# Kernel optimization log

Measured on AMD Instinct MI355X. Metric: run time of the kernel, lower is better.

The kernel has to match this reference:

```python
import jax, jax.numpy as jnp
import numpy as np

NEG_INF = -1e38


def wkv(k, v, w, u):
    """Log-sum-exp-stabilized RWKV WKV scan.
    k, v: (B, T, C); w, u: (C,). Returns y: (B, T, C).
    """
    B, T, C = k.shape

    def step(carry, kv_t):
        num, den, mx = carry            # each (B, C)
        k_t, v_t = kv_t                 # (B, C)
        ku = k_t + u
        m = jnp.maximum(mx, ku)
        e1 = jnp.exp(mx - m)
        e2 = jnp.exp(ku - m)
        y = (e1 * num + e2 * v_t) / (e1 * den + e2)
        # state update
        mw = mx + w
        m2 = jnp.maximum(mw, k_t)
        es1 = jnp.exp(mw - m2)
        es2 = jnp.exp(k_t - m2)
        num = es1 * num + es2 * v_t
        den = es1 * den + es2
        return (num, den, m2), y

    init = (jnp.zeros((B, C), k.dtype),
            jnp.zeros((B, C), k.dtype),
            jnp.full((B, C), NEG_INF, k.dtype))
    _, y = jax.lax.scan(step, init, (jnp.swapaxes(k, 0, 1), jnp.swapaxes(v, 0, 1)))
    return jnp.swapaxes(y, 0, 1)


def setup_inputs() -> dict:
    key = jax.random.key(0)
    ks = jax.random.split(key, 8)
    B, T, C = 8, 4096, 512
    x = jax.random.normal(ks[0], (B, T, C), dtype=jnp.float32)
    # Linear weights stored as (in, out) so forward is x @ W.
    W_rkv = jax.random.normal(ks[1], (C, 6 * C), dtype=jnp.float32) / np.sqrt(C)
    W_out = jax.random.normal(ks[2], (2 * C, C), dtype=jnp.float32) / np.sqrt(2 * C)
    time_decay = jax.random.uniform(ks[3], (C,), minval=-6.0, maxval=-5.0, dtype=jnp.float32)
    time_first = jax.random.uniform(ks[4], (C,), minval=-3.0, maxval=0.0, dtype=jnp.float32)
    time_decay_rev = jax.random.uniform(ks[5], (C,), minval=-6.0, maxval=-5.0, dtype=jnp.float32)
    time_first_rev = jax.random.uniform(ks[6], (C,), minval=-3.0, maxval=0.0, dtype=jnp.float32)
    return {"x": x, "W_rkv": W_rkv, "W_out": W_out,
            "time_decay": time_decay, "time_first": time_first,
            "time_decay_rev": time_decay_rev, "time_first_rev": time_first_rev}


def reference(x, W_rkv, W_out, time_decay, time_first, time_decay_rev, time_first_rev):
    B, T, C = x.shape
    rkv = (x @ W_rkv).reshape(B, T, 2, 3, C)
    # forward direction
    r_f, k_f, v_f = rkv[:, :, 0, 0], rkv[:, :, 0, 1], rkv[:, :, 0, 2]
    w_f = -jnp.exp(time_decay)
    out_f = jax.nn.sigmoid(r_f) * wkv(k_f, v_f, w_f, time_first)
    # backward direction (run scan on time-reversed k/v, then reverse back)
    r_b, k_b, v_b = rkv[:, :, 1, 0], rkv[:, :, 1, 1], rkv[:, :, 1, 2]
    w_b = -jnp.exp(time_decay_rev)
    out_b = wkv(k_b[:, ::-1], v_b[:, ::-1], w_b, time_first_rev)[:, ::-1]
    out_b = jax.nn.sigmoid(r_b) * out_b
    out_cat = jnp.concatenate([out_f, out_b], axis=-1)  # (B, T, 2C)
    return out_cat @ W_out
```

## Files before the change

### kernel.cpp

```cpp
#include <hip/hip_runtime.h>

typedef float f4 __attribute__((ext_vector_type(4)));
typedef unsigned short us4 __attribute__((ext_vector_type(4)));
typedef __bf16 bf16x8 __attribute__((ext_vector_type(8)));
typedef float f32x4 __attribute__((ext_vector_type(4)));
typedef _Float16 h8 __attribute__((ext_vector_type(8)));

#define TT 4096
#define CCH 512
#define NCH2 256
#define CHL2 16
#define NSEG 32
#define SEGC 8

__device__ __forceinline__ unsigned short f2bf(float f) {
  unsigned u = __builtin_bit_cast(unsigned, f);
  unsigned r = (u + 0x7FFFu + ((u >> 16) & 1u)) >> 16;
  return (unsigned short)r;
}
__device__ __forceinline__ void gload_lds16(const void* g, void* l) {
  __builtin_amdgcn_global_load_lds(
      (const __attribute__((address_space(1))) unsigned int*)g,
      (__attribute__((address_space(3))) unsigned int*)l, 16, 0, 0);
}
#define VMCNT(n) asm volatile("s_waitcnt vmcnt(" #n ")" ::: "memory")

__global__ __launch_bounds__(256)
void convert_f32_bf16(const float* __restrict__ in, unsigned short* __restrict__ out, int n4) {
  int i = blockIdx.x * 256 + threadIdx.x;
  if (i >= n4) return;
  f4 f = *(const f4*)(in + (size_t)i * 4);
  us4 o = { f2bf(f[0]), f2bf(f[1]), f2bf(f[2]), f2bf(f[3]) };
  *(us4*)(out + (size_t)i * 4) = o;
}

__global__ __launch_bounds__(256)
void transpose_to_bf16(const float* __restrict__ in, unsigned short* __restrict__ out,
                       int R, int Cc) {
  __shared__ unsigned short tile[32][33];
  int c0 = blockIdx.x * 32, r0 = blockIdx.y * 32;
  int tx = threadIdx.x, ty = threadIdx.y;
  #pragma unroll
  for (int j = 0; j < 32; j += 8)
    tile[ty + j][tx] = f2bf(in[(size_t)(r0 + ty + j) * Cc + c0 + tx]);
  __syncthreads();
  #pragma unroll
  for (int j = 0; j < 32; j += 8)
    out[(size_t)(c0 + ty + j) * R + r0 + tx] = tile[tx][ty + j];
}

__global__ __launch_bounds__(256)
void transpose_to_f16(const float* __restrict__ in, _Float16* __restrict__ out,
                      int R, int Cc) {
  __shared__ _Float16 tile[32][33];
  int c0 = blockIdx.x * 32, r0 = blockIdx.y * 32;
  int tx = threadIdx.x, ty = threadIdx.y;
  #pragma unroll
  for (int j = 0; j < 32; j += 8)
    tile[ty + j][tx] = (_Float16)in[(size_t)(r0 + ty + j) * Cc + c0 + tx];
  __syncthreads();
  #pragma unroll
  for (int j = 0; j < 32; j += 8)
    out[(size_t)(c0 + ty + j) * R + r0 + tx] = tile[tx][ty + j];
}

__global__ __launch_bounds__(512, 2)
void gemm256_g1(const unsigned short* __restrict__ A,
                const unsigned short* __restrict__ BT,
                _Float16* __restrict__ kbuf, _Float16* __restrict__ vbuf,
                _Float16* __restrict__ rbuf) {
  __shared__ char lds[131072];
  const int tid = threadIdx.x;
  const int lane = tid & 63, wv = tid >> 6;
  const int wm = wv >> 2, wn = wv & 3;
  const int ln15 = lane & 15, lq = lane >> 4;

  const int nwg = gridDim.x;
  const int bid = blockIdx.x;
  const int wgid = (nwg % 8 == 0) ? (bid % 8) * (nwg / 8) + bid / 8 : bid;
  const int bn = wgid % 12, bm = wgid / 12;
  const size_t m0 = (size_t)bm * 256, n0 = (size_t)bn * 256;
  const char* Ab = (const char*)(A + m0 * 512);
  const char* Bb = (const char*)(BT + n0 * 512);

  const int srow0 = tid >> 2, srow1 = 128 + (tid >> 2);
  const int sg = tid & 3;
  const int sgs0 = (sg ^ ((srow0 >> 1) & 3)) << 4;
  const int sgs1 = (sg ^ ((srow1 >> 1) & 3)) << 4;

  auto STAGE = [&](int mat, int t, int h) {
    const char* gsrc = mat ? Bb : Ab;
    char* ldst = lds + mat * 65536 + ((t & 1) << 15) + (h << 14);
    const size_t co = (size_t)t * 128 + (size_t)h * 64;
    gload_lds16(gsrc + (size_t)srow0 * 1024 + co + sgs0, ldst + tid * 16);
    gload_lds16(gsrc + (size_t)srow1 * 1024 + co + sgs1, ldst + 8192 + tid * 16);
  };

  f32x4 acc[8][4] = {};
  STAGE(0, 0, 0); STAGE(1, 0, 0); STAGE(0, 0, 1); STAGE(1, 0, 1);

  for (int t = 0; t < 8; ++t) {
    char* Abase = lds + ((t & 1) << 15);
    char* Bbase = lds + 65536 + ((t & 1) << 15);
    VMCNT(4);
    __builtin_amdgcn_s_barrier();
    __builtin_amdgcn_sched_barrier(0);
    {
      bf16x8 bf[4], af[8];
      #pragma unroll
      for (int fn = 0; fn < 4; ++fn) {
        const int r = wn * 64 + fn * 16 + ln15;
        bf[fn] = *(const bf16x8*)(Bbase + r * 64 + ((lq ^ ((r >> 1) & 3)) << 4));
      }
      #pragma unroll
      for (int fm = 0; fm < 8; ++fm) {
        const int r = wm * 128 + fm * 16 + ln15;
        af[fm] = *(const bf16x8*)(Abase + r * 64 + ((lq ^ ((r >> 1) & 3)) << 4));
      }
      if (t < 7) { STAGE(0, t + 1, 0); STAGE(1, t + 1, 0); }
      __builtin_amdgcn_s_setprio(1);
      #pragma unroll
      for (int fm = 0; fm < 8; ++fm)
        #pragma unroll
        for (int fn = 0; fn < 4; ++fn)
          acc[fm][fn] = __builtin_amdgcn_mfma_f32_16x16x32_bf16(af[fm], bf[fn], acc[fm][fn], 0, 0, 0);
      __builtin_amdgcn_s_setprio(0);
    }
    if (t < 7) { VMCNT(4); } else { VMCNT(0); }
    __builtin_amdgcn_s_barrier();
    __builtin_amdgcn_sched_barrier(0);
    {
      bf16x8 bf[4], af[8];
      #pragma unroll
      for (int fn = 0; fn < 4; ++fn) {
        const int r = wn * 64 + fn * 16 + ln15;
        bf[fn] = *(const bf16x8*)(Bbase + 16384 + r * 64 + ((lq ^ ((r >> 1) & 3)) << 4));
      }
      #pragma unroll
      for (int fm = 0; fm < 8; ++fm) {
        const int r = wm * 128 + fm * 16 + ln15;
        af[fm] = *(const bf16x8*)(Abase + 16384 + r * 64 + ((lq ^ ((r >> 1) & 3)) << 4));
      }
      if (t < 7) { STAGE(0, t + 1, 1); STAGE(1, t + 1, 1); }
      __builtin_amdgcn_s_setprio(1);
      #pragma unroll
      for (int fm = 0; fm < 8; ++fm)
        #pragma unroll
        for (int fn = 0; fn < 4; ++fn)
          acc[fm][fn] = __builtin_amdgcn_mfma_f32_16x16x32_bf16(af[fm], bf[fn], acc[fm][fn], 0, 0, 0);
      __builtin_amdgcn_s_setprio(0);
    }
  }

  const int n0i = (int)n0;
  const int dir = (n0i >= 1536) ? 1 : 0;
  const int jj0 = n0i - dir * 1536;
  const int seg = jj0 >> 9;
  const int cbase = jj0 & 511;
  _Float16* dbuf = (seg == 0) ? rbuf : (seg == 1 ? kbuf : vbuf);
  float* stg = (float*)lds;
  const int ebnd = wv >> 2;
  const int erow = (tid >> 3) & 31;
  const int el8 = tid & 7;
  __syncthreads();
  #pragma unroll
  for (int gi = 0; gi < 4; ++gi) {
    #pragma unroll
    for (int f2 = 0; f2 < 2; ++f2) {
      const int fm = gi * 2 + f2;
      #pragma unroll
      for (int q = 0; q < 4; ++q) {
        const int rloc = f2 * 16 + lq * 4 + q;
        float* dst = stg + wm * 8192 + rloc * 256;
        const int sw = ((rloc >> 2) & 1) << 4;
        #pragma unroll
        for (int fn = 0; fn < 4; ++fn)
          dst[(wn * 64 + fn * 16 + ln15) ^ sw] = acc[fm][fn][q];
      }
    }
    __syncthreads();
    {
      const int rowg = (int)m0 + ebnd * 128 + gi * 32 + erow;
      const int b_ = rowg >> 12, tt = rowg & 4095;
      const int trow = dir ? (4095 - tt) : tt;
      _Float16* gp = dbuf + ((size_t)(b_ * 2 + dir) * TT + trow) * 512 + cbase;
      const float* sp = stg + ebnd * 8192 + erow * 256;
      const int sw = ((erow >> 2) & 1) << 4;
      #pragma unroll
      for (int u = 0; u < 4; ++u) {
        const int cf = el8 * 8 + u * 64;
        const int cs = cf ^ sw;
        f4 a = *(const f4*)(sp + cs);
        f4 b = *(const f4*)(sp + cs + 4);
        h8 hv = { (_Float16)a[0], (_Float16)a[1], (_Float16)a[2], (_Float16)a[3],
                  (_Float16)b[0], (_Float16)b[1], (_Float16)b[2], (_Float16)b[3] };
        *(h8*)(gp + cf) = hv;
      }
    }
    __syncthreads();
  }
}

__global__ __launch_bounds__(256)
void gemm2_k(const _Float16* __restrict__ obuf,
             const _Float16* __restrict__ BT,
             int M, float* __restrict__ out) {
  __shared__ char smem[16384];
  _Float16* As  = (_Float16*)smem;
  _Float16* Bsm = (_Float16*)(smem + 8192);
  const int tid = threadIdx.x;
  const int lane = tid & 63, wv = tid >> 6;
  const int wr = wv >> 1, wc = wv & 1;
  const int ln15 = lane & 15, lq = lane >> 4;
  const int mtiles = M >> 7;
  const int bm = blockIdx.x % mtiles, bn = blockIdx.x / mtiles;
  const size_t m0 = (size_t)bm << 7, n0 = (size_t)bn << 7;
  f32x4 acc[4][4] = {};
  const int bB = (int)(m0 >> 12);
  const int tbase = (int)(m0 & 4095);
  const char* Bb = (const char*)(BT + n0 * 1024);
  const int r0 = tid >> 2;
  const int cb = (((tid & 3) ^ (r0 & 3)) << 4);

  for (int k0 = 0; k0 < 1024; k0 += 32) {
    const int half = k0 >> 9;
    const size_t kb = (size_t)(k0 & 511) * 2;
    const char* Ah = (const char*)(obuf + ((size_t)(bB * 2 + half) << 12) * 512);
    const size_t ar0 = half ? (size_t)(4095 - (tbase + r0))      : (size_t)(tbase + r0);
    const size_t ar1 = half ? (size_t)(4095 - (tbase + r0 + 64)) : (size_t)(tbase + r0 + 64);
    gload_lds16(Ah + ar0 * 1024 + kb + cb, (char*)As + tid * 16);
    gload_lds16(Ah + ar1 * 1024 + kb + cb, (char*)As + 4096 + tid * 16);
    gload_lds16(Bb + (size_t)r0 * 2048 + (size_t)k0 * 2 + cb,        (char*)Bsm + tid * 16);
    gload_lds16(Bb + (size_t)(r0 + 64) * 2048 + (size_t)k0 * 2 + cb, (char*)Bsm + 4096 + tid * 16);
    __syncthreads();
    h8 af[4], bg[4];
    #pragma unroll
    for (int i = 0; i < 4; ++i) {
      const int ar = wr * 64 + i * 16 + ln15;
      const int br = wc * 64 + i * 16 + ln15;
      af[i] = *(const h8*)((char*)As  + ((ar * 4 + (lq ^ (ar & 3))) << 4));
      bg[i] = *(const h8*)((char*)Bsm + ((br * 4 + (lq ^ (br & 3))) << 4));
    }
    #pragma unroll
    for (int i = 0; i < 4; ++i)
      #pragma unroll
      for (int j = 0; j < 4; ++j)
        acc[i][j] = __builtin_amdgcn_mfma_f32_16x16x32_f16(af[i], bg[j], acc[i][j], 0, 0, 0);
    __syncthreads();
  }

  const int tq = tid >> 3, t8 = tid & 7;
  #pragma unroll
  for (int i = 0; i < 4; ++i) {
    __syncthreads();
    float* st = (float*)smem;
    #pragma unroll
    for (int j = 0; j < 4; ++j) {
      const int cl = wc * 64 + j * 16 + ln15;
      #pragma unroll
      for (int q = 0; q < 4; ++q) {
        const int rl = wr * 16 + lq * 4 + q;
        st[rl * 128 + (cl ^ (((rl >> 2) & 3) << 4))] = acc[i][j][q];
      }
    }
    __syncthreads();
    const int rl = tq, lqp = (rl >> 2) & 3;
    const int lr = ((rl >> 4) << 6) + (i << 4) + (rl & 15);
    const int rowg = (int)m0 + lr;
    #pragma unroll
    for (int u = 0; u < 4; ++u) {
      const int colL = t8 * 16 + u * 4;
      const int colS = colL ^ (lqp << 4);
      f4 vv = *(const f4*)(st + rl * 128 + colS);
      *(f4*)(out + (size_t)rowg * 512 + n0 + colL) = vv;
    }
  }
}

__global__ __launch_bounds__(128)
void wkv_pass1(const _Float16* __restrict__ kbuf, const _Float16* __restrict__ vbuf,
               const float* __restrict__ td, const float* __restrict__ tdr,
               float* __restrict__ cN, float* __restrict__ cD, float* __restrict__ cM) {
  const int bd = blockIdx.x;
  const int ch = blockIdx.y * 2 + threadIdx.y;
  const int dir = bd & 1;
  const int c = threadIdx.x * 8;
  const float* tdp = (dir ? tdr : td) + c;
  float w[8], num[8], den[8], m[8];
  #pragma unroll
  for (int e = 0; e < 8; ++e) { w[e] = -__expf(tdp[e]); num[e] = 0.f; den[e] = 0.f; m[e] = -1e38f; }
  const size_t base = ((size_t)bd * TT + (size_t)ch * CHL2) * CCH + c;
  const _Float16* kp = kbuf + base;
  const _Float16* vp = vbuf + base;
  h8 ka = *(const h8*)(kp), va = *(const h8*)(vp);
  h8 kb = *(const h8*)(kp + CCH), vb = *(const h8*)(vp + CCH);
  for (int t = 0; t < CHL2; ++t) {
    h8 kc = {}, vc = {};
    if (t + 2 < CHL2) {
      kc = *(const h8*)(kp + (size_t)(t + 2) * CCH);
      vc = *(const h8*)(vp + (size_t)(t + 2) * CCH);
    }
    #pragma unroll
    for (int e = 0; e < 8; ++e) {
      float ke = (float)ka[e], ve = (float)va[e];
      float mw = m[e] + w[e];
      float m2 = fmaxf(mw, ke);
      float e1 = __expf(mw - m2), e2 = __expf(ke - m2);
      num[e] = e1 * num[e] + e2 * ve;
      den[e] = e1 * den[e] + e2;
      m[e] = m2;
    }
    ka = kb; va = vb; kb = kc; vb = vc;
  }
  const size_t ci = ((size_t)bd * NCH2 + ch) * CCH + c;
  #pragma unroll
  for (int h = 0; h < 2; ++h) {
    *(f4*)(cN + ci + h * 4) = (f4){num[h*4], num[h*4+1], num[h*4+2], num[h*4+3]};
    *(f4*)(cD + ci + h * 4) = (f4){den[h*4], den[h*4+1], den[h*4+2], den[h*4+3]};
    *(f4*)(cM + ci + h * 4) = (f4){m[h*4], m[h*4+1], m[h*4+2], m[h*4+3]};
  }
}

__global__ __launch_bounds__(128)
void wkv_p2a(const float* __restrict__ td, const float* __restrict__ tdr,
             const float* __restrict__ cN, const float* __restrict__ cD,
             const float* __restrict__ cM,
             float* __restrict__ scN, float* __restrict__ scD, float* __restrict__ scM) {
  const int bd = blockIdx.x, seg = blockIdx.y;
  const int dir = bd & 1;
  const int c = threadIdx.x * 4;
  f4 tdv = *(const f4*)((dir ? tdr : td) + c);
  float dw[4], num[4], den[4], m[4];
  #pragma unroll
  for (int e = 0; e < 4; ++e) { dw[e] = -__expf(tdv[e]) * (float)CHL2; num[e] = 0.f; den[e] = 0.f; m[e] = -1e38f; }
  size_t ci = ((size_t)bd * NCH2 + (size_t)seg * SEGC) * CCH + c;
  for (int j = 0; j < SEGC; ++j, ci += CCH) {
    f4 ln = *(const f4*)(cN + ci);
    f4 ld = *(const f4*)(cD + ci);
    f4 lm = *(const f4*)(cM + ci);
    #pragma unroll
    for (int e = 0; e < 4; ++e) {
      float mp = m[e] + dw[e];
      float mm = fmaxf(mp, lm[e]);
      float e1 = __expf(mp - mm), e2 = __expf(lm[e] - mm);
      num[e] = e1 * num[e] + e2 * ln[e];
      den[e] = e1 * den[e] + e2 * ld[e];
      m[e] = mm;
    }
  }
  const size_t si = ((size_t)bd * NSEG + seg) * CCH + c;
  *(f4*)(scN + si) = (f4){num[0], num[1], num[2], num[3]};
  *(f4*)(scD + si) = (f4){den[0], den[1], den[2], den[3]};
  *(f4*)(scM + si) = (f4){m[0], m[1], m[2], m[3]};
}

__global__ __launch_bounds__(128)
void wkv_p2b(const float* __restrict__ td, const float* __restrict__ tdr,
             float* __restrict__ scN, float* __restrict__ scD, float* __restrict__ scM) {
  const int bd = blockIdx.x;
  const int dir = bd & 1;
  const int c = threadIdx.x * 4;
  f4 tdv = *(const f4*)((dir ? tdr : td) + c);
  float dws[4], num[4], den[4], m[4];
  #pragma unroll
  for (int e = 0; e < 4; ++e) { dws[e] = -__expf(tdv[e]) * (float)(CHL2 * SEGC); num[e] = 0.f; den[e] = 0.f; m[e] = -1e38f; }
  size_t si = (size_t)bd * NSEG * CCH + c;
  for (int s = 0; s < NSEG; ++s, si += CCH) {
    f4 ln = *(const f4*)(scN + si);
    f4 ld = *(const f4*)(scD + si);
    f4 lm = *(const f4*)(scM + si);
    *(f4*)(scN + si) = (f4){num[0], num[1], num[2], num[3]};
    *(f4*)(scD + si) = (f4){den[0], den[1], den[2], den[3]};
    *(f4*)(scM + si) = (f4){m[0], m[1], m[2], m[3]};
    #pragma unroll
    for (int e = 0; e < 4; ++e) {
      float mp = m[e] + dws[e];
      float mm = fmaxf(mp, lm[e]);
      float e1 = __expf(mp - mm), e2 = __expf(lm[e] - mm);
      num[e] = e1 * num[e] + e2 * ln[e];
      den[e] = e1 * den[e] + e2 * ld[e];
      m[e] = mm;
    }
  }
}

__global__ __launch_bounds__(128)
void wkv_p2c(const float* __restrict__ td, const float* __restrict__ tdr,
             const float* __restrict__ scN, const float* __restrict__ scD,
             const float* __restrict__ scM,
             float* __restrict__ cN, float* __restrict__ cD, float* __restrict__ cM) {
  const int bd = blockIdx.x, seg = blockIdx.y;
  const int dir = bd & 1;
  const int c = threadIdx.x * 4;
  f4 tdv = *(const f4*)((dir ? tdr : td) + c);
  const size_t si = ((size_t)bd * NSEG + seg) * CCH + c;
  f4 nv = *(const f4*)(scN + si);
  f4 dv = *(const f4*)(scD + si);
  f4 mv = *(const f4*)(scM + si);
  float dw[4], num[4], den[4], m[4];
  #pragma unroll
  for (int e = 0; e < 4; ++e) {
    dw[e] = -__expf(tdv[e]) * (float)CHL2;
    num[e] = nv[e]; den[e] = dv[e]; m[e] = mv[e];
  }
  size_t ci = ((size_t)bd * NCH2 + (size_t)seg * SEGC) * CCH + c;
  for (int j = 0; j < SEGC; ++j, ci += CCH) {
    f4 ln = *(const f4*)(cN + ci);
    f4 ld = *(const f4*)(cD + ci);
    f4 lm = *(const f4*)(cM + ci);
    *(f4*)(cN + ci) = (f4){num[0], num[1], num[2], num[3]};
    *(f4*)(cD + ci) = (f4){den[0], den[1], den[2], den[3]};
    *(f4*)(cM + ci) = (f4){m[0], m[1], m[2], m[3]};
    #pragma unroll
    for (int e = 0; e < 4; ++e) {
      float mp = m[e] + dw[e];
      float mm = fmaxf(mp, lm[e]);
      float e1 = __expf(mp - mm), e2 = __expf(lm[e] - mm);
      num[e] = e1 * num[e] + e2 * ln[e];
      den[e] = e1 * den[e] + e2 * ld[e];
      m[e] = mm;
    }
  }
}

__global__ __launch_bounds__(128)
void wkv_pass3(const _Float16* __restrict__ kbuf, const _Float16* __restrict__ vbuf,
               _Float16* __restrict__ rbuf,
               const float* __restrict__ td, const float* __restrict__ tf,
               const float* __restrict__ tdr, const float* __restrict__ tfr,
               const float* __restrict__ cN, const float* __restrict__ cD,
               const float* __restrict__ cM) {
  const int bd = blockIdx.x;
  const int ch = blockIdx.y * 2 + threadIdx.y;
  const int dir = bd & 1;
  const int c = threadIdx.x * 8;
  const float* tdp = (dir ? tdr : td) + c;
  const float* tup = (dir ? tfr : tf) + c;
  const size_t ci = ((size_t)bd * NCH2 + ch) * CCH + c;
  float w[8], u[8], num[8], den[8], m[8];
  #pragma unroll
  for (int e = 0; e < 8; ++e) {
    w[e] = -__expf(tdp[e]); u[e] = tup[e];
    num[e] = cN[ci + e]; den[e] = cD[ci + e]; m[e] = cM[ci + e];
  }
  const size_t base = ((size_t)bd * TT + (size_t)ch * CHL2) * CCH + c;
  const _Float16* kp = kbuf + base;
  const _Float16* vp = vbuf + base;
  _Float16* rp = rbuf + base;
  h8 ka = *(const h8*)(kp), va = *(const h8*)(vp), ra = *(const h8*)(rp);
  h8 kb = *(const h8*)(kp + CCH), vb = *(const h8*)(vp + CCH), rb = *(const h8*)(rp + CCH);
  for (int t = 0; t < CHL2; ++t) {
    h8 kc = {}, vc = {}, rc = {};
    if (t + 2 < CHL2) {
      kc = *(const h8*)(kp + (size_t)(t + 2) * CCH);
      vc = *(const h8*)(vp + (size_t)(t + 2) * CCH);
      rc = *(const h8*)(rp + (size_t)(t + 2) * CCH);
    }
    _Float16 o[8];
    #pragma unroll
    for (int e = 0; e < 8; ++e) {
      float ke = (float)ka[e], ve = (float)va[e];
      float ku = ke + u[e];
      float mm = fmaxf(m[e], ku);
      float e1 = __expf(m[e] - mm), e2 = __expf(ku - mm);
      float y = (e1 * num[e] + e2 * ve) * __builtin_amdgcn_rcpf(e1 * den[e] + e2);
      float rt = (float)ra[e];
      float sig = __builtin_amdgcn_rcpf(1.f + __expf(-rt));
      o[e] = (_Float16)(sig * y);
      float mw = m[e] + w[e];
      float m2 = fmaxf(mw, ke);
      float es1 = __expf(mw - m2), es2 = __expf(ke - m2);
      num[e] = es1 * num[e] + es2 * ve;
      den[e] = es1 * den[e] + es2;
      m[e] = m2;
    }
    h8 ov = { o[0], o[1], o[2], o[3], o[4], o[5], o[6], o[7] };
    *(h8*)(rp + (size_t)t * CCH) = ov;
    ka = kb; va = vb; ra = rb; kb = kc; vb = vc; rb = rc;
  }
}

extern "C" void kernel_launch(void* const* d_in, const int* in_sizes, int n_in,
                              void* d_out, int out_size, void* d_ws, size_t ws_size,
                              hipStream_t stream) {
  const float* x   = (const float*)d_in[0];
  const float* Wr  = (const float*)d_in[1];
  const float* Wo  = (const float*)d_in[2];
  const float* td  = (const float*)d_in[3];
  const float* tf  = (const float*)d_in[4];
  const float* tdr = (const float*)d_in[5];
  const float* tfr = (const float*)d_in[6];
  float* out = (float*)d_out;

  auto rnd = [](size_t b) { return (b + 255) & ~(size_t)255; };
  const size_t wBytes = rnd((size_t)3072 * 512 * 2) + rnd((size_t)512 * 1024 * 2);
  auto need = [&](int Bs) {
    size_t s = wBytes;
    s += 3 * rnd((size_t)Bs * 2 * TT * 512 * 2);
    s += rnd((size_t)Bs * TT * 512 * 2);
    return s;
  };
  int Bs = 8;
  while (Bs > 1 && need(Bs) > ws_size) Bs >>= 1;

  char* ws = (char*)d_ws;
  size_t off = 0;
  auto alloc = [&](size_t bytes) -> char* {
    char* p = ws + off;
    off += (bytes + 255) & ~(size_t)255;
    return p;
  };
  unsigned short* wrkvT = (unsigned short*)alloc((size_t)3072 * 512 * 2);
  _Float16*       woutT = (_Float16*)alloc((size_t)512 * 1024 * 2);
  _Float16*       kbuf  = (_Float16*)alloc((size_t)Bs * 2 * TT * 512 * 2);
  _Float16*       vbuf  = (_Float16*)alloc((size_t)Bs * 2 * TT * 512 * 2);
  _Float16*       rbuf  = (_Float16*)alloc((size_t)Bs * 2 * TT * 512 * 2);
  unsigned short* xb    = (unsigned short*)alloc((size_t)Bs * TT * 512 * 2);
  const size_t cs = (size_t)Bs * 2 * NCH2 * 512;
  const size_t ss = (size_t)Bs * 2 * NSEG * 512;
  float* cN  = (float*)xb;
  float* cD  = cN + cs;
  float* cM  = cD + cs;
  float* scN = cM + cs;
  float* scD = scN + ss;
  float* scM = scD + ss;

  transpose_to_bf16<<<dim3(3072 / 32, 512 / 32), dim3(32, 8), 0, stream>>>(Wr, wrkvT, 512, 3072);
  transpose_to_f16<<<dim3(512 / 32, 1024 / 32), dim3(32, 8), 0, stream>>>(Wo, woutT, 1024, 512);

  const int nslices = 8 / Bs;
  const int Mslice = Bs * TT;
  const int mt256 = Mslice >> 8;
  const int mt128 = Mslice >> 7;
  for (int s = 0; s < nslices; ++s) {
    const float* xs = x + (size_t)s * Mslice * 512;
    float* outs = out + (size_t)s * Mslice * 512;
    convert_f32_bf16<<<Mslice * 512 / 1024, 256, 0, stream>>>(xs, xb, Mslice * 512 / 4);
    gemm256_g1<<<mt256 * 12, 512, 0, stream>>>(xb, wrkvT, kbuf, vbuf, rbuf);
    wkv_pass1<<<dim3(Bs * 2, NCH2 / 2), dim3(64, 2), 0, stream>>>(kbuf, vbuf, td, tdr, cN, cD, cM);
    wkv_p2a<<<dim3(Bs * 2, NSEG), 128, 0, stream>>>(td, tdr, cN, cD, cM, scN, scD, scM);
    wkv_p2b<<<Bs * 2, 128, 0, stream>>>(td, tdr, scN, scD, scM);
    wkv_p2c<<<dim3(Bs * 2, NSEG), 128, 0, stream>>>(td, tdr, scN, scD, scM, cN, cD, cM);
    wkv_pass3<<<dim3(Bs * 2, NCH2 / 2), dim3(64, 2), 0, stream>>>(kbuf, vbuf, rbuf, td, tf, tdr, tfr,
                                                                  cN, cD, cM);
    gemm2_k<<<mt128 * 4, 256, 0, stream>>>(rbuf, woutT, Mslice, outs);
  }
}
```

Baseline: 334.3 us.

## Replace output GEMM with 256x256 tile, double-buffered LDS pipelined kernel

Replaces the 128x128 single-buffered output projection GEMM with a 256x256-tile, 512-thread kernel. It stages 64-wide K chunks in two halves, double-buffers them in LDS, and overlaps global-to-LDS loads with MFMA using vmcnt waits and s_setprio. It also remaps workgroup IDs so neighbouring blocks land on different XCDs, and uses a wider swizzled epilogue. The aim is more data reuse per tile and less load latency exposed in the K loop. The cost is 128KB of LDS and heavy register use, which limits occupancy. The grid also becomes small (two N tiles), which may underfill the CUs.

```diff
diff --git a/kernel.cpp b/kernel.cpp
--- a/kernel.cpp
+++ b/kernel.cpp
@@ -201,79 +201,140 @@
   }
 }
 
-__global__ __launch_bounds__(256)
-void gemm2_k(const _Float16* __restrict__ obuf,
-             const _Float16* __restrict__ BT,
-             int M, float* __restrict__ out) {
-  __shared__ char smem[16384];
-  _Float16* As  = (_Float16*)smem;
-  _Float16* Bsm = (_Float16*)(smem + 8192);
+__global__ __launch_bounds__(512, 2)
+void gemm2_256(const _Float16* __restrict__ obuf,
+               const _Float16* __restrict__ BT,
+               float* __restrict__ out) {
+  __shared__ char lds[131072];
   const int tid = threadIdx.x;
   const int lane = tid & 63, wv = tid >> 6;
-  const int wr = wv >> 1, wc = wv & 1;
+  const int wm = wv >> 2, wn = wv & 3;
   const int ln15 = lane & 15, lq = lane >> 4;
-  const int mtiles = M >> 7;
-  const int bm = blockIdx.x % mtiles, bn = blockIdx.x / mtiles;
-  const size_t m0 = (size_t)bm << 7, n0 = (size_t)bn << 7;
-  f32x4 acc[4][4] = {};
+
+  const int nwg = gridDim.x;
+  const int bid = blockIdx.x;
+  const int wgid = (nwg % 8 == 0) ? (bid % 8) * (nwg / 8) + bid / 8 : bid;
+  const int bn = wgid % 2, bm = wgid / 2;
+  const size_t m0 = (size_t)bm * 256, n0 = (size_t)bn * 256;
   const int bB = (int)(m0 >> 12);
   const int tbase = (int)(m0 & 4095);
   const char* Bb = (const char*)(BT + n0 * 1024);
-  const int r0 = tid >> 2;
-  const int cb = (((tid & 3) ^ (r0 & 3)) << 4);
-
-  for (int k0 = 0; k0 < 1024; k0 += 32) {
-    const int half = k0 >> 9;
-    const size_t kb = (size_t)(k0 & 511) * 2;
-    const char* Ah = (const char*)(obuf + ((size_t)(bB * 2 + half) << 12) * 512);
-    const size_t ar0 = half ? (size_t)(4095 - (tbase + r0))      : (size_t)(tbase + r0);
-    const size_t ar1 = half ? (size_t)(4095 - (tbase + r0 + 64)) : (size_t)(tbase + r0 + 64);
-    gload_lds16(Ah + ar0 * 1024 + kb + cb, (char*)As + tid * 16);
-    gload_lds16(Ah + ar1 * 1024 + kb + cb, (char*)As + 4096 + tid * 16);
-    gload_lds16(Bb + (size_t)r0 * 2048 + (size_t)k0 * 2 + cb,        (char*)Bsm + tid * 16);
-    gload_lds16(Bb + (size_t)(r0 + 64) * 2048 + (size_t)k0 * 2 + cb, (char*)Bsm + 4096 + tid * 16);
+
+  const int srow0 = tid >> 2, srow1 = 128 + (tid >> 2);
+  const int sg = tid & 3;
+  const int sgs0 = (sg ^ ((srow0 >> 1) & 3)) << 4;
+  const int sgs1 = (sg ^ ((srow1 >> 1) & 3)) << 4;
+
+  auto STAGE = [&](int mat, int t, int h) {
+    char* ldst = lds + mat * 65536 + ((t & 1) << 15) + (h << 14);
+    if (mat == 0) {
+      const int half = t >> 3;
+      const char* Ah = (const char*)(obuf + (((size_t)(bB * 2 + half)) << 12) * 512);
+      const size_t co = (size_t)(t & 7) * 128 + (size_t)h * 64;
+      const size_t ar0 = half ? (size_t)(4095 - (tbase + srow0)) : (size_t)(tbase + srow0);
+      const size_t ar1 = half ? (size_t)(4095 - (tbase + srow1)) : (size_t)(tbase + srow1);
+      gload_lds16(Ah + ar0 * 1024 + co + sgs0, ldst + tid * 16);
+      gload_lds16(Ah + ar1 * 1024 + co + sgs1, ldst + 8192 + tid * 16);
+    } else {
+      const size_t co = (size_t)t * 128 + (size_t)h * 64;
+      gload_lds16(Bb + (size_t)srow0 * 2048 + co + sgs0, ldst + tid * 16);
+      gload_lds16(Bb + (size_t)srow1 * 2048 + co + sgs1, ldst + 8192 + tid * 16);
+    }
+  };
+
+  f32x4 acc[8][4] = {};
+  STAGE(0, 0, 0); STAGE(1, 0, 0); STAGE(0, 0, 1); STAGE(1, 0, 1);
+
+  for (int t = 0; t < 16; ++t) {
+    char* Abase = lds + ((t & 1) << 15);
+    char* Bbase = lds + 65536 + ((t & 1) << 15);
+    VMCNT(4);
+    __builtin_amdgcn_s_barrier();
+    __builtin_amdgcn_sched_barrier(0);
+    {
+      h8 bf[4], af[8];
+      #pragma unroll
+      for (int fn = 0; fn < 4; ++fn) {
+        const int r = wn * 64 + fn * 16 + ln15;
+        bf[fn] = *(const h8*)(Bbase + r * 64 + ((lq ^ ((r >> 1) & 3)) << 4));
+      }
+      #pragma unroll
+      for (int fm = 0; fm < 8; ++fm) {
+        const int r = wm * 128 + fm * 16 + ln15;
+        af[fm] = *(const h8*)(Abase + r * 64 + ((lq ^ ((r >> 1) & 3)) << 4));
+      }
+      if (t < 15) { STAGE(0, t + 1, 0); STAGE(1, t + 1, 0); }
+      __builtin_amdgcn_s_setprio(1);
+      #pragma unroll
+      for (int fm = 0; fm < 8; ++fm)
+        #pragma unroll
+        for (int fn = 0; fn < 4; ++fn)
+          acc[fm][fn] = __builtin_amdgcn_mfma_f32_16x16x32_f16(af[fm], bf[fn], acc[fm][fn], 0, 0, 0);
+      __builtin_amdgcn_s_setprio(0);
+    }
+    if (t < 15) { VMCNT(4); } else { VMCNT(0); }
+    __builtin_amdgcn_s_barrier();
+    __builtin_amdgcn_sched_barrier(0);
+    {
+      h8 bf[4], af[8];
+      #pragma unroll
+      for (int fn = 0; fn < 4; ++fn) {
+        const int r = wn * 64 + fn * 16 + ln15;
+        bf[fn] = *(const h8*)(Bbase + 16384 + r * 64 + ((lq ^ ((r >> 1) & 3)) << 4));
+      }
+      #pragma unroll
+      for (int fm = 0; fm < 8; ++fm) {
+        const int r = wm * 128 + fm * 16 + ln15;
+        af[fm] = *(const h8*)(Abase + 16384 + r * 64 + ((lq ^ ((r >> 1) & 3)) << 4));
+      }
+      if (t < 15) { STAGE(0, t + 1, 1); STAGE(1, t + 1, 1); }
+      __builtin_amdgcn_s_setprio(1);
+      #pragma unroll
+      for (int fm = 0; fm < 8; ++fm)
+        #pragma unroll
+        for (int fn = 0; fn < 4; ++fn)
+          acc[fm][fn] = __builtin_amdgcn_mfma_f32_16x16x32_f16(af[fm], bf[fn], acc[fm][fn], 0, 0, 0);
+      __builtin_amdgcn_s_setprio(0);
+    }
+  }
+
+  float* stg = (float*)lds;
+  const int ebnd = wv >> 2;
+  const int erow = (tid >> 3) & 31;
+  const int el8 = tid & 7;
+  __syncthreads();
+  #pragma unroll
+  for (int gi = 0; gi < 4; ++gi) {
+    #pragma unroll
+    for (int f2 = 0; f2 < 2; ++f2) {
+      const int fm = gi * 2 + f2;
+      #pragma unroll
+      for (int q = 0; q < 4; ++q) {
+        const int rloc = f2 * 16 + lq * 4 + q;
+        float* dst = stg + wm * 8192 + rloc * 256;
+        const int sw = ((rloc >> 2) & 1) << 4;
+        #pragma unroll
+        for (int fn = 0; fn < 4; ++fn)
+          dst[(wn * 64 + fn * 16 + ln15) ^ sw] = acc[fm][fn][q];
+      }
+    }
     __syncthreads();
-    h8 af[4], bg[4];
-    #pragma unroll
-    for (int i = 0; i < 4; ++i) {
-      const int ar = wr * 64 + i * 16 + ln15;
-      const int br = wc * 64 + i * 16 + ln15;
-      af[i] = *(const h8*)((char*)As  + ((ar * 4 + (lq ^ (ar & 3))) << 4));
-      bg[i] = *(const h8*)((char*)Bsm + ((br * 4 + (lq ^ (br & 3))) << 4));
-    }
-    #pragma unroll
-    for (int i = 0; i < 4; ++i)
-      #pragma unroll
-      for (int j = 0; j < 4; ++j)
-        acc[i][j] = __builtin_amdgcn_mfma_f32_16x16x32_f16(af[i], bg[j], acc[i][j], 0, 0, 0);
+    {
+      const int rowg = (int)m0 + ebnd * 128 + gi * 32 + erow;
+      float* gp = out + (size_t)rowg * 512 + n0;
+      const float* sp = stg + ebnd * 8192 + erow * 256;
+      const int sw = ((erow >> 2) & 1) << 4;
+      #pragma unroll
+      for (int u = 0; u < 4; ++u) {
+        const int cf = el8 * 8 + u * 64;
+        const int cs = cf ^ sw;
+        f4 a = *(const f4*)(sp + cs);
+        f4 b = *(const f4*)(sp + cs + 4);
+        *(f4*)(gp + cf) = a;
+        *(f4*)(gp + cf + 4) = b;
+      }
+    }
     __syncthreads();
-  }
-
-  const int tq = tid >> 3, t8 = tid & 7;
-  #pragma unroll
-  for (int i = 0; i < 4; ++i) {
-    __syncthreads();
-    float* st = (float*)smem;
-    #pragma unroll
-    for (int j = 0; j < 4; ++j) {
-      const int cl = wc * 64 + j * 16 + ln15;
-      #pragma unroll
-      for (int q = 0; q < 4; ++q) {
-        const int rl = wr * 16 + lq * 4 + q;
-        st[rl * 128 + (cl ^ (((rl >> 2) & 3) << 4))] = acc[i][j][q];
-      }
-    }
-    __syncthreads();
-    const int rl = tq, lqp = (rl >> 2) & 3;
-    const int lr = ((rl >> 4) << 6) + (i << 4) + (rl & 15);
-    const int rowg = (int)m0 + lr;
-    #pragma unroll
-    for (int u = 0; u < 4; ++u) {
-      const int colL = t8 * 16 + u * 4;
-      const int colS = colL ^ (lqp << 4);
-      f4 vv = *(const f4*)(st + rl * 128 + colS);
-      *(f4*)(out + (size_t)rowg * 512 + n0 + colL) = vv;
-    }
   }
 }
 
@@ -531,7 +592,6 @@
   const int nslices = 8 / Bs;
   const int Mslice = Bs * TT;
   const int mt256 = Mslice >> 8;
-  const int mt128 = Mslice >> 7;
   for (int s = 0; s < nslices; ++s) {
     const float* xs = x + (size_t)s * Mslice * 512;
     float* outs = out + (size_t)s * Mslice * 512;
@@ -543,6 +603,6 @@
     wkv_p2c<<<dim3(Bs * 2, NSEG), 128, 0, stream>>>(td, tdr, scN, scD, scM, cN, cD, cM);
     wkv_pass3<<<dim3(Bs * 2, NCH2 / 2), dim3(64, 2), 0, stream>>>(kbuf, vbuf, rbuf, td, tf, tdr, tfr,
                                                                   cN, cD, cM);
-    gemm2_k<<<mt128 * 4, 256, 0, stream>>>(rbuf, woutT, Mslice, outs);
-  }
-}
+    gemm2_256<<<mt256 * 2, 512, 0, stream>>>(rbuf, woutT, outs);
+  }
+}
```

Measured after the change: 301.1 us, median of 3. 9.9% less time.
